# Kernel tuning notes

Measured on AMD Instinct MI355X. Metric: run time of the kernel, lower is better.

The kernel has to match this reference:

```python
import jax, jax.numpy as jnp
import numpy as np

N_NODES = 100000
N_EDGES = 1600000
H = 64
EPS_SM = 1e-16
NEG_SLOPE = 0.01  # LeakyReLU default
BN_EPS = 1e-5


def leaky_relu(x):
    return jnp.where(x >= 0, x, NEG_SLOPE * x)


def transformer_conv(x, src, tgt, edge_attr, Wq, bq, Wk, bk, Wv, bv, We, Ws, bs):
    # PyG TransformerConv, heads=1, concat=True, root_weight=True, lin_edge bias=False
    n = x.shape[0]
    q = x @ Wq + bq            # [N,H]
    k = x @ Wk + bk            # [N,H]
    v = x @ Wv + bv            # [N,H]
    e = edge_attr @ We         # [E,H]
    ke = k[src] + e            # [E,H]
    score = jnp.sum(q[tgt] * ke, axis=-1) / jnp.sqrt(jnp.float32(H))  # [E]
    # segment softmax over incoming edges of each target node
    m = jax.ops.segment_max(score, tgt, num_segments=n)
    m = jnp.where(jnp.isfinite(m), m, 0.0)
    p = jnp.exp(score - m[tgt])
    denom = jax.ops.segment_sum(p, tgt, num_segments=n)
    alpha = p / (denom[tgt] + EPS_SM)
    msg = (v[src] + e) * alpha[:, None]                  # [E,H]
    out = jax.ops.segment_sum(msg, tgt, num_segments=n)  # [N,H]
    return out + x @ Ws + bs


def batch_norm(x, gamma, beta):
    mean = jnp.mean(x, axis=0)
    var = jnp.mean((x - mean) ** 2, axis=0)
    return (x - mean) / jnp.sqrt(var + BN_EPS) * gamma + beta


def setup_inputs() -> dict:
    key = jax.random.key(0)
    ks = jax.random.split(key, 24)
    s = 0.05
    d = {
        "x": jax.random.normal(ks[0], (N_NODES, 2), jnp.float32),
        "edge_index": jax.random.randint(ks[1], (2, N_EDGES), 0, N_NODES, jnp.int32),
        "edge_attr": jax.random.normal(ks[2], (N_EDGES, 2), jnp.float32),
        "mask": jax.random.uniform(ks[3], (N_NODES,), jnp.float32),
        # gcn1 (in=2)
        "Wq1": jax.random.normal(ks[4], (2, H)) * s, "bq1": jnp.zeros((H,)),
        "Wk1": jax.random.normal(ks[5], (2, H)) * s, "bk1": jnp.zeros((H,)),
        "Wv1": jax.random.normal(ks[6], (2, H)) * s, "bv1": jnp.zeros((H,)),
        "We1": jax.random.normal(ks[7], (2, H)) * s,
        "Ws1": jax.random.normal(ks[8], (2, H)) * s, "bs1": jnp.zeros((H,)),
        # gcn2 (in=64)
        "Wq2": jax.random.normal(ks[9], (H, H)) * s, "bq2": jnp.zeros((H,)),
        "Wk2": jax.random.normal(ks[10], (H, H)) * s, "bk2": jnp.zeros((H,)),
        "Wv2": jax.random.normal(ks[11], (H, H)) * s, "bv2": jnp.zeros((H,)),
        "We2": jax.random.normal(ks[12], (2, H)) * s,
        "Ws2": jax.random.normal(ks[13], (H, H)) * s, "bs2": jnp.zeros((H,)),
        # batch norm
        "bn_gamma": jnp.ones((H,)), "bn_beta": jnp.zeros((H,)),
        # final MLP 64->32->1
        "Wf1": jax.random.normal(ks[14], (H, 32)) * s, "bf1": jnp.zeros((32,)),
        "Wf2": jax.random.normal(ks[15], (32, 1)) * s, "bf2": jnp.zeros((1,)),
        "iterations": 3,
    }
    return d


def reference(x, edge_index, edge_attr, mask,
              Wq1, bq1, Wk1, bk1, Wv1, bv1, We1, Ws1, bs1,
              Wq2, bq2, Wk2, bk2, Wv2, bv2, We2, Ws2, bs2,
              bn_gamma, bn_beta, Wf1, bf1, Wf2, bf2, iterations):
    src, tgt = edge_index[0], edge_index[1]
    h = transformer_conv(x, src, tgt, edge_attr, Wq1, bq1, Wk1, bk1, Wv1, bv1, We1, Ws1, bs1)
    h = leaky_relu(batch_norm(h, bn_gamma, bn_beta))
    h = leaky_relu(transformer_conv(h, src, tgt, edge_attr, Wq2, bq2, Wk2, bk2, Wv2, bv2, We2, Ws2, bs2))
    for _ in range(iterations - 1):
        h = leaky_relu(transformer_conv(h, src, tgt, edge_attr, Wq2, bq2, Wk2, bk2, Wv2, bv2, We2, Ws2, bs2))
    out = jnp.squeeze(leaky_relu(h @ Wf1 + bf1) @ Wf2 + bf2, axis=-1)  # [N]
    return out * mask
```

## Files before the change

kernel.cpp:

```cpp
#include <hip/hip_runtime.h>
#include <hip/hip_fp16.h>

#define N_NODES 100000
#define N_EDGES 1600000
#define SCAN_B ((N_NODES + 1023) / 1024)
#define BSHIFT 7
#define NB_BKT ((N_NODES + 127) / 128)
#define BCAP 2560

typedef _Float16 half2_t __attribute__((ext_vector_type(2)));
typedef _Float16 half8_t __attribute__((ext_vector_type(8)));
typedef float f32x4 __attribute__((ext_vector_type(4)));

__device__ __forceinline__ float lrelu(float x) { return x >= 0.f ? x : 0.01f * x; }

__global__ void k_count(const int* __restrict__ tgt, int* __restrict__ deg) {
    int i = blockIdx.x * 256 + threadIdx.x;
    atomicAdd(&deg[tgt[i]], 1);
}

__global__ void k_scan1(const int* __restrict__ deg, int* __restrict__ bsum) {
    __shared__ int s[256];
    int t = threadIdx.x;
    int gi = blockIdx.x * 1024 + t * 4;
    int v = 0;
    if (gi < N_NODES) {
        int4 d = *(const int4*)&deg[gi];
        v = d.x + d.y + d.z + d.w;
    }
    s[t] = v;
    __syncthreads();
    for (int d = 128; d > 0; d >>= 1) {
        if (t < d) s[t] += s[t + d];
        __syncthreads();
    }
    if (t == 0) bsum[blockIdx.x] = s[0];
}

__global__ void k_scan2(int* bsum, int* rowptr) {
    if (threadIdx.x == 0) {
        int run = 0;
        for (int b = 0; b < SCAN_B; b++) {
            int v = bsum[b];
            bsum[b] = run;
            run += v;
        }
        rowptr[N_NODES] = run;
    }
}

__global__ void k_scan3(const int* __restrict__ deg, const int* __restrict__ bsum,
                        int* __restrict__ rowptr, int* __restrict__ fill) {
    __shared__ int s[256];
    int t = threadIdx.x;
    int gi = blockIdx.x * 1024 + t * 4;
    int4 d = make_int4(0, 0, 0, 0);
    if (gi < N_NODES) d = *(const int4*)&deg[gi];
    int tsum = d.x + d.y + d.z + d.w;
    s[t] = tsum;
    __syncthreads();
    for (int dd = 1; dd < 256; dd <<= 1) {
        int val = (t >= dd) ? s[t - dd] : 0;
        __syncthreads();
        s[t] += val;
        __syncthreads();
    }
    int texcl = s[t] - tsum + bsum[blockIdx.x];
    if (gi < N_NODES) {
        int4 w;
        w.x = texcl;
        w.y = texcl + d.x;
        w.z = texcl + d.x + d.y;
        w.w = texcl + d.x + d.y + d.z;
        *(int4*)&rowptr[gi] = w;
        *(int4*)&fill[gi] = w;
    }
}

__global__ void k_scatter(const int* __restrict__ src, const int* __restrict__ tgt,
                          const float2* __restrict__ ea,
                          int* __restrict__ fill, int2* __restrict__ csr) {
    int i = blockIdx.x * 256 + threadIdx.x;
    int t = tgt[i];
    float2 e = ea[i];
    int pos = atomicAdd(&fill[t], 1);
    __half2 h2 = __floats2half2_rn(e.x, e.y);
    csr[pos] = make_int2(src[i], *(int*)&h2);
}

__global__ __launch_bounds__(256) void k_bin1(const int* __restrict__ src,
                                              const int* __restrict__ tgt,
                                              const float2* __restrict__ ea,
                                              int* __restrict__ gCur,
                                              int2* __restrict__ bin) {
    __shared__ int hist[NB_BKT];
    __shared__ int cur[NB_BKT];
    int tid = threadIdx.x;
    for (int b = tid; b < NB_BKT; b += 256) hist[b] = 0;
    __syncthreads();
    int base = blockIdx.x * 6400;
#pragma unroll 5
    for (int k = 0; k < 25; k++) {
        int i = base + k * 256 + tid;
        atomicAdd(&hist[tgt[i] >> BSHIFT], 1);
    }
    __syncthreads();
    for (int b = tid; b < NB_BKT; b += 256)
        cur[b] = atomicAdd(&gCur[b], hist[b]);
    __syncthreads();
    for (int k = 0; k < 25; k++) {
        int i = base + k * 256 + tid;
        int t = tgt[i];
        int b = t >> BSHIFT;
        float2 e = ea[i];
        int pos = atomicAdd(&cur[b], 1);
        if (pos < BCAP) {
            __half2 h2 = __floats2half2_rn(e.x, e.y);
            int2 rec;
            rec.x = src[i] | ((t & 127) << 20);
            rec.y = *(int*)&h2;
            bin[(size_t)b * BCAP + pos] = rec;
        }
    }
}

__global__ __launch_bounds__(256) void k_bin2(const int* __restrict__ gCnt,
                                              const int2* __restrict__ bin,
                                              int2* __restrict__ csr,
                                              int* __restrict__ fill) {
    __shared__ int cnt[128];
    int tid = threadIdx.x;
    if (tid < 128) cnt[tid] = 0;
    __syncthreads();
    int b = blockIdx.x;
    int nb = min(gCnt[b], BCAP);
    const int2* myb = &bin[(size_t)b * BCAP];
    for (int i = tid; i < nb; i += 256) {
        int2 rec = myb[i];
        int tloc = (rec.x >> 20) & 127;
        int s = rec.x & 0xFFFFF;
        int pos = atomicAdd(&cnt[tloc], 1);
        if (pos < 64) {
            int node = (b << BSHIFT) + tloc;
            csr[((size_t)node << 6) + pos] = make_int2(s | (rec.x & 0xFFF00000), rec.y);
        }
    }
    __syncthreads();
    if (tid < 128) {
        int node = (b << BSHIFT) + tid;
        if (node < N_NODES) fill[node] = min(cnt[tid], 64);
    }
}

__global__ void k_prep2(const float* __restrict__ Wq, const float* __restrict__ Wk,
                        const float* __restrict__ Ws, const float* __restrict__ We,
                        const float* __restrict__ bk, float* __restrict__ Wcomb) {
    int idx = blockIdx.x * 256 + threadIdx.x;
    if (idx >= 9216) return;
    int j = idx / 144;
    int m = idx - j * 144;
    float v = 0.f;
    if (m < 64) {
        float s = 0.f;
        for (int ch = 0; ch < 64; ch++) s += Wq[j * 64 + ch] * Wk[m * 64 + ch];
        v = 0.125f * s;
    } else if (m < 128) {
        v = Ws[j * 64 + (m - 64)];
    } else if (m == 128) {
        float s = 0.f;
        for (int ch = 0; ch < 64; ch++) s += Wq[j * 64 + ch] * bk[ch];
        v = 0.125f * s;
    } else if (m <= 130) {
        float s = 0.f;
        for (int ch = 0; ch < 64; ch++) s += Wq[j * 64 + ch] * We[(m - 129) * 64 + ch];
        v = 0.125f * s;
    }
    Wcomb[idx] = v;
}

__global__ void k_prepb(const float* __restrict__ Wk2, const float* __restrict__ We2,
                        const float* __restrict__ bq2, const float* __restrict__ bk2,
                        const float* __restrict__ bs2, const float* __restrict__ Wq1,
                        const float* __restrict__ Wk1, const float* __restrict__ We1,
                        const float* __restrict__ bq1, const float* __restrict__ bk1,
                        float* __restrict__ bcomb) {
    int t = threadIdx.x;
    if (t >= 160) return;
    float v = 0.f;
    if (t < 64) {
        float s = 0.f;
        for (int i = 0; i < 64; i++) s += Wk2[t * 64 + i] * bq2[i];
        v = 0.125f * s;
    } else if (t < 128) {
        v = bs2[t - 64];
    } else if (t == 128) {
        float s = 0.f;
        for (int i = 0; i < 64; i++) s += bq2[i] * bk2[i];
        v = 0.125f * s;
    } else if (t <= 130) {
        float s = 0.f;
        for (int i = 0; i < 64; i++) s += bq2[i] * We2[(t - 129) * 64 + i];
        v = 0.125f * s;
    } else if (t < 144) {
        v = 0.f;
    } else {
        int t2 = t - 144;
        float s = 0.f;
        if (t2 < 4) {
            int j = t2 >> 1, m = t2 & 1;
            for (int ch = 0; ch < 64; ch++) s += Wq1[j * 64 + ch] * Wk1[m * 64 + ch];
        } else if (t2 < 6) {
            int j = t2 - 4;
            for (int ch = 0; ch < 64; ch++) s += Wq1[j * 64 + ch] * bk1[ch];
        } else if (t2 < 8) {
            int m = t2 - 6;
            for (int ch = 0; ch < 64; ch++) s += bq1[ch] * Wk1[m * 64 + ch];
        } else if (t2 == 8) {
            for (int ch = 0; ch < 64; ch++) s += bq1[ch] * bk1[ch];
        } else if (t2 < 13) {
            int j = (t2 - 9) >> 1, d = (t2 - 9) & 1;
            for (int ch = 0; ch < 64; ch++) s += Wq1[j * 64 + ch] * We1[d * 64 + ch];
        } else if (t2 < 15) {
            int d = t2 - 13;
            for (int ch = 0; ch < 64; ch++) s += bq1[ch] * We1[d * 64 + ch];
        }
        v = 0.125f * s;
    }
    bcomb[t] = v;
}

__global__ void k_prepw(const float* __restrict__ Wcomb, __half* __restrict__ wp) {
    int t = blockIdx.x * 256 + threadIdx.x;
    if (t >= 9216) return;
    int e = t & 7;
    int lane = (t >> 3) & 63;
    int kh = (t >> 9) & 1;
    int fm = t >> 10;
    int k = (kh << 5) + ((lane >> 4) << 3) + e;
    int c = fm * 16 + (lane & 15);
    wp[t] = __float2half(Wcomb[k * 144 + c]);
}

__global__ void k_prepv(const float* __restrict__ Wv, __half* __restrict__ wvp) {
    int t = blockIdx.x * 256 + threadIdx.x;
    if (t >= 4096) return;
    int e = t & 7;
    int lane = (t >> 3) & 63;
    int kh = (t >> 9) & 1;
    int fm = t >> 10;
    int k = (kh << 5) + ((lane >> 4) << 3) + e;
    int c = fm * 16 + (lane & 15);
    wvp[t] = __float2half(Wv[k * 64 + c]);
}

__global__ __launch_bounds__(256) void k_agg1(
    const float* __restrict__ x, const int* __restrict__ idx,
    const int2* __restrict__ csr, const float* __restrict__ Wv,
    const float* __restrict__ We, const float* __restrict__ Ws,
    const float* __restrict__ bv, const float* __restrict__ bs,
    const float* __restrict__ prep, __half* __restrict__ oh, int bucket) {
    int node = blockIdx.x * 4 + (threadIdx.x >> 6);
    int lane = threadIdx.x & 63;
    float2 xt = *(const float2*)&x[(size_t)node << 1];
    float a0 = xt.x * prep[0] + xt.y * prep[2] + prep[6];
    float a1 = xt.x * prep[1] + xt.y * prep[3] + prep[7];
    float b1 = xt.x * prep[4] + xt.y * prep[5] + prep[8];
    float g0 = xt.x * prep[9] + xt.y * prep[11] + prep[13];
    float g1 = xt.x * prep[10] + xt.y * prep[12] + prep[14];

    float l = 0.f, px0 = 0.f, px1 = 0.f, pA = 0.f, pB = 0.f;
    if (bucket) {
        int deg = idx[node];
        bool valid = lane < deg;
        int2 rec = valid ? csr[((size_t)node << 6) + lane] : make_int2(0, 0);
        int src = rec.x & 0xFFFFF;
        float2 ef = __half22float2(*(__half2*)&rec.y);
        float2 xs = valid ? *(const float2*)&x[(size_t)src << 1] : make_float2(0.f, 0.f);
        float t = a0 * xs.x + a1 * xs.y + b1 + g0 * ef.x + g1 * ef.y;
        float pp = valid ? __expf(t) : 0.f;
        l = pp;
        px0 = pp * xs.x;
        px1 = pp * xs.y;
        pA = pp * ef.x;
        pB = pp * ef.y;
    } else {
        int beg = idx[node], end = idx[node + 1];
        for (int p = beg + lane; p < end; p += 64) {
            int2 rec = csr[p];
            float2 ef = __half22float2(*(__half2*)&rec.y);
            float2 xs = *(const float2*)&x[(size_t)rec.x << 1];
            float t = a0 * xs.x + a1 * xs.y + b1 + g0 * ef.x + g1 * ef.y;
            float pp = __expf(t);
            l += pp;
            px0 += pp * xs.x;
            px1 += pp * xs.y;
            pA += pp * ef.x;
            pB += pp * ef.y;
        }
    }
#pragma unroll
    for (int D = 1; D < 64; D <<= 1) {
        l += __shfl_xor(l, D, 64);
        px0 += __shfl_xor(px0, D, 64);
        px1 += __shfl_xor(px1, D, 64);
        pA += __shfl_xor(pA, D, 64);
        pB += __shfl_xor(pB, D, 64);
    }
    float inv = 1.f / (l + 1e-16f);
    int c = lane;
    float r = (px0 * Wv[c] + px1 * Wv[64 + c] + pA * We[c] + pB * We[64 + c] +
               l * bv[c]) * inv +
              xt.x * Ws[c] + xt.y * Ws[64 + c] + bs[c];
    oh[((size_t)node << 6) + c] = __float2half(r);
}

__global__ void k_bnp(const __half* __restrict__ oh, float* __restrict__ bnsum,
                      float* __restrict__ bnsq) {
    __shared__ float s1[256], s2[256];
    int t = threadIdx.x;
    int c = t & 63, nsub = t >> 6;
    float su = 0.f, sq = 0.f;
    int base = blockIdx.x * 400;
    for (int i = 0; i < 100; i++) {
        int node = base + i * 4 + nsub;
        float v = __half2float(oh[((size_t)node << 6) + c]);
        su += v;
        sq += v * v;
    }
    s1[t] = su;
    s2[t] = sq;
    __syncthreads();
    if (t < 64) {
        float a = s1[t] + s1[t + 64] + s1[t + 128] + s1[t + 192];
        float b = s2[t] + s2[t + 64] + s2[t + 128] + s2[t + 192];
        atomicAdd(&bnsum[t], a);
        atomicAdd(&bnsq[t], b);
    }
}

__global__ void k_bnf(const float* bnsum, const float* bnsq, const float* gamma,
                      const float* beta, float* bnab) {
    int c = threadIdx.x;
    float mean = bnsum[c] * (1.f / N_NODES);
    float var = bnsq[c] * (1.f / N_NODES) - mean * mean;
    float A = gamma[c] * rsqrtf(var + 1e-5f);
    bnab[c] = A;
    bnab[64 + c] = beta[c] - mean * A;
}

__global__ void k_bna(const __half* __restrict__ oh, const float* __restrict__ bnab,
                      __half* __restrict__ hh) {
    int idx = blockIdx.x * 256 + threadIdx.x;
    int c = idx & 63;
    float v = lrelu(__half2float(oh[idx]) * bnab[c] + bnab[64 + c]);
    hh[idx] = __float2half(v);
}

__global__ __launch_bounds__(256) void k_gemm(
    const __half* __restrict__ oh, const __half* __restrict__ hhin,
    const __half* __restrict__ wp, const float* __restrict__ bcomb,
    const float* __restrict__ bnab, int use_bn,
    __half* __restrict__ qh, float* __restrict__ ext, __half* __restrict__ hhout) {
    __shared__ __half qsm[64 * 68];
    int tid = threadIdx.x;
    int w = tid >> 6;
    int lane = tid & 63;
    int nloc = lane & 15;
    int kg = lane >> 4;
    int base = blockIdx.x * 64;

    half8_t A[2], AE[2];
    const half8_t* wpv = (const half8_t*)wp;
#pragma unroll
    for (int kh = 0; kh < 2; kh++) A[kh] = wpv[((w << 1) + kh) * 64 + lane];
    if (w == 3) {
#pragma unroll
        for (int kh = 0; kh < 2; kh++) AE[kh] = wpv[((8 << 1) + kh) * 64 + lane];
    }

    half8_t z8;
#pragma unroll
    for (int i = 0; i < 8; i++) z8[i] = (_Float16)0.f;

    half8_t B[4][2];
    int n[4];
    bool g[4];
#pragma unroll
    for (int nf = 0; nf < 4; nf++) {
        n[nf] = base + (nf << 4) + nloc;
        g[nf] = n[nf] < N_NODES;
    }

    if (use_bn) {
        float4 bnA[2][2], bnB[2][2];
#pragma unroll
        for (int kh = 0; kh < 2; kh++) {
            int k0 = (kh << 5) + (kg << 3);
            bnA[kh][0] = *(const float4*)&bnab[k0];
            bnA[kh][1] = *(const float4*)&bnab[k0 + 4];
            bnB[kh][0] = *(const float4*)&bnab[64 + k0];
            bnB[kh][1] = *(const float4*)&bnab[64 + k0 + 4];
        }
        const int4 zi4 = make_int4(0, 0, 0, 0);
#pragma unroll
        for (int nf = 0; nf < 4; nf++) {
            const __half* orow = oh + ((size_t)n[nf] << 6);
#pragma unroll
            for (int kh = 0; kh < 2; kh++) {
                int k0 = (kh << 5) + (kg << 3);
                int4 raw = g[nf] ? *(const int4*)&orow[k0] : zi4;
                const __half2* op = (const __half2*)&raw;
                float2 o01 = __half22float2(op[0]);
                float2 o23 = __half22float2(op[1]);
                float2 o45 = __half22float2(op[2]);
                float2 o67 = __half22float2(op[3]);
                float4 lo, hi;
                lo.x = lrelu(o01.x * bnA[kh][0].x + bnB[kh][0].x);
                lo.y = lrelu(o01.y * bnA[kh][0].y + bnB[kh][0].y);
                lo.z = lrelu(o23.x * bnA[kh][0].z + bnB[kh][0].z);
                lo.w = lrelu(o23.y * bnA[kh][0].w + bnB[kh][0].w);
                hi.x = lrelu(o45.x * bnA[kh][1].x + bnB[kh][1].x);
                hi.y = lrelu(o45.y * bnA[kh][1].y + bnB[kh][1].y);
                hi.z = lrelu(o67.x * bnA[kh][1].z + bnB[kh][1].z);
                hi.w = lrelu(o67.y * bnA[kh][1].w + bnB[kh][1].w);
                half8_t r;
                r[0] = (_Float16)lo.x; r[1] = (_Float16)lo.y;
                r[2] = (_Float16)lo.z; r[3] = (_Float16)lo.w;
                r[4] = (_Float16)hi.x; r[5] = (_Float16)hi.y;
                r[6] = (_Float16)hi.z; r[7] = (_Float16)hi.w;
                B[nf][kh] = r;
                if (g[nf]) *(half8_t*)&hhout[((size_t)n[nf] << 6) + k0] = r;
            }
        }
    } else {
#pragma unroll
        for (int nf = 0; nf < 4; nf++) {
#pragma unroll
            for (int kh = 0; kh < 2; kh++) {
                int k0 = (kh << 5) + (kg << 3);
                B[nf][kh] = g[nf] ? *(const half8_t*)&hhin[((size_t)n[nf] << 6) + k0]
                                  : z8;
            }
        }
    }

    f32x4 acc[4], accE[4];
#pragma unroll
    for (int nf = 0; nf < 4; nf++) {
        acc[nf] = (f32x4){0.f, 0.f, 0.f, 0.f};
        accE[nf] = (f32x4){0.f, 0.f, 0.f, 0.f};
    }

#pragma unroll
    for (int nf = 0; nf < 4; nf++) {
        acc[nf] = __builtin_amdgcn_mfma_f32_16x16x32_f16(A[0], B[nf][0], acc[nf],
                                                          0, 0, 0);
        acc[nf] = __builtin_amdgcn_mfma_f32_16x16x32_f16(A[1], B[nf][1], acc[nf],
                                                          0, 0, 0);
    }
    if (w == 3) {
#pragma unroll
        for (int nf = 0; nf < 4; nf++) {
            accE[nf] = __builtin_amdgcn_mfma_f32_16x16x32_f16(AE[0], B[nf][0],
                                                              accE[nf], 0, 0, 0);
            accE[nf] = __builtin_amdgcn_mfma_f32_16x16x32_f16(AE[1], B[nf][1],
                                                              accE[nf], 0, 0, 0);
        }
    }

    int rowg = kg << 2;
    int c0 = (w << 4) + rowg;
    float4 bi = *(const float4*)&bcomb[c0];
#pragma unroll
    for (int nf = 0; nf < 4; nf++) {
        int nl = (nf << 4) + nloc;
        __half2 p0 = __floats2half2_rn(acc[nf][0] + bi.x, acc[nf][1] + bi.y);
        __half2 p1 = __floats2half2_rn(acc[nf][2] + bi.z, acc[nf][3] + bi.w);
        *(__half2*)&qsm[nl * 68 + c0] = p0;
        *(__half2*)&qsm[nl * 68 + c0 + 2] = p1;
    }
    if (w == 3 && kg == 0) {
        float4 be = *(const float4*)&bcomb[128];
#pragma unroll
        for (int nf = 0; nf < 4; nf++) {
            if (!g[nf]) continue;
            float4 r;
            r.x = accE[nf][0] + be.x;
            r.y = accE[nf][1] + be.y;
            r.z = accE[nf][2] + be.z;
            r.w = accE[nf][3] + be.w;
            *(float4*)&ext[(size_t)n[nf] << 2] = r;
        }
    }
    __syncthreads();
#pragma unroll
    for (int rep = 0; rep < 8; rep++) {
        int i = rep * 256 + tid;
        int row = i >> 5;
        int col = (i & 31) << 1;
        if (base + row < N_NODES) {
            int v = *(int*)&qsm[row * 68 + col];
            *(int*)&qh[((size_t)(base + row) << 6) + col] = v;
        }
    }
}

__global__ __launch_bounds__(256) void k_fused(
    __half* qh, float* ext,
    const __half* __restrict__ hh_in, __half* __restrict__ hh_out,
    const int* __restrict__ idx, const int2* __restrict__ csr,
    const __half* __restrict__ wp, const __half* __restrict__ wvp,
    const float* __restrict__ We, const float* __restrict__ bv,
    const float* __restrict__ bcomb,
    const float* __restrict__ Wf1, const float* __restrict__ bf1,
    const float* __restrict__ Wf2, const float* __restrict__ bf2v,
    const float* __restrict__ mask, float* __restrict__ out,
    int last, int bucket) {
    __shared__ __align__(16) char smem[20480 + 9216 + 1024];
    float* red = (float*)smem;
    __half* rsm16 = (__half*)smem;
    float* rsm32 = (float*)smem;
    __half* Shatsm = (__half*)(smem + 20480);
    __half* qsm = (__half*)(smem + 20480);
    float* W1sm = (float*)(smem + 20480);
    float4* svecsm = (float4*)(smem + 20480 + 9216);

    int tid = threadIdx.x;
    int wv = tid >> 6;
    int lane = tid & 63;
    int base = blockIdx.x * 64;

    {
        int es = lane >> 2, cl = lane & 3;
        float* myred = &red[(wv * 64 + lane) * 20];
        int rb = wv * 64 * 20 + (lane >> 4) * 20 + (lane & 15);
        for (int nl = 0; nl < 16; nl++) {
            int node = base + (wv << 4) + nl;
            if (node >= N_NODES) continue;
            float4 ex = *(const float4*)&ext[(size_t)node << 2];
            float beta = ex.x, qe0 = ex.y, qe1 = ex.z;
            int4 qr0 = *(const int4*)&qh[((size_t)node << 6) + (cl << 4)];
            int4 qr1 = *(const int4*)&qh[((size_t)node << 6) + (cl << 4) + 8];
            const half2_t* qp0 = (const half2_t*)&qr0;
            const half2_t* qp1 = (const half2_t*)&qr1;

            float l = 0.f, sA = 0.f, sB = 0.f;
            float accv[16];
#pragma unroll
            for (int c = 0; c < 16; c++) accv[c] = 0.f;

            int nEdge, rbase2;
            if (bucket) {
                nEdge = idx[node];
                rbase2 = node << 6;
            } else {
                rbase2 = idx[node];
                nEdge = idx[node + 1] - rbase2;
            }
            int nIter = (nEdge + 15) >> 4;

            auto body = [&](int4 h0, int4 h1, int2 rec, bool ok) {
                const half2_t* hp0 = (const half2_t*)&h0;
                const half2_t* hp1 = (const half2_t*)&h1;
                float t = 0.f;
#if __has_builtin(__builtin_amdgcn_fdot2)
#pragma unroll
                for (int p = 0; p < 4; p++)
                    t = __builtin_amdgcn_fdot2(hp0[p], qp0[p], t, false);
#pragma unroll
                for (int p = 0; p < 4; p++)
                    t = __builtin_amdgcn_fdot2(hp1[p], qp1[p], t, false);
#else
                const __half* hq0 = (const __half*)&qr0;
                const __half* hq1 = (const __half*)&qr1;
                const __half* hh0 = (const __half*)&h0;
                const __half* hh1 = (const __half*)&h1;
#pragma unroll
                for (int c = 0; c < 8; c++)
                    t += __half2float(hh0[c]) * __half2float(hq0[c]);
#pragma unroll
                for (int c = 0; c < 8; c++)
                    t += __half2float(hh1[c]) * __half2float(hq1[c]);
#endif
                t += __shfl_xor(t, 1, 64);
                t += __shfl_xor(t, 2, 64);
                float2 ef = __half22float2(*(__half2*)&rec.y);
                t += beta + ef.x * qe0 + ef.y * qe1;
                float pp = ok ? __expf(t) : 0.f;
                l += pp;
                sA += pp * ef.x;
                sB += pp * ef.y;
                const __half* hs0 = (const __half*)&h0;
                const __half* hs1 = (const __half*)&h1;
#pragma unroll
                for (int c = 0; c < 8; c++) accv[c] += pp * __half2float(hs0[c]);
#pragma unroll
                for (int c = 0; c < 8; c++) accv[8 + c] += pp * __half2float(hs1[c]);
            };

            if (bucket) {
                int2 recs[4];
#pragma unroll
                for (int i = 0; i < 4; i++) {
                    int e = (i << 4) + es;
                    recs[i] = (e < nEdge) ? csr[(size_t)rbase2 + e] : make_int2(0, 0);
                }
                if (nIter > 0) {
                    int src0 = recs[0].x & 0xFFFFF;
                    const __half* hr = hh_in + ((size_t)src0 << 6) + (cl << 4);
                    int4 h0c = *(const int4*)&hr[0];
                    int4 h1c = *(const int4*)&hr[8];
#pragma unroll
                    for (int i = 0; i < 4; i++) {
                        if (i < nIter) {
                            int4 h0 = h0c, h1 = h1c;
                            if (i + 1 < nIter) {
                                int srcn = recs[i + 1].x & 0xFFFFF;
                                const __half* hrn =
                                    hh_in + ((size_t)srcn << 6) + (cl << 4);
                                h0c = *(const int4*)&hrn[0];
                                h1c = *(const int4*)&hrn[8];
                            }
                            body(h0, h1, recs[i], ((i << 4) + es) < nEdge);
                        }
                    }
                }
            } else {
                for (int i = 0; i < nIter; i++) {
                    int e = (i << 4) + es;
                    bool ok = e < nEdge;
                    int2 rec = ok ? csr[(size_t)rbase2 + e] : make_int2(0, 0);
                    int src = rec.x & 0xFFFFF;
                    const __half* hr = hh_in + ((size_t)src << 6) + (cl << 4);
                    int4 h0 = *(const int4*)&hr[0];
                    int4 h1 = *(const int4*)&hr[8];
                    body(h0, h1, rec, ok);
                }
            }

#pragma unroll
            for (int D = 4; D < 64; D <<= 1) {
                l += __shfl_xor(l, D, 64);
                sA += __shfl_xor(sA, D, 64);
                sB += __shfl_xor(sB, D, 64);
            }
            float inv = 1.f / (l + 1e-16f);

#pragma unroll
            for (int c = 0; c < 16; c += 4)
                *(float4*)&myred[c] =
                    make_float4(accv[c], accv[c + 1], accv[c + 2], accv[c + 3]);
            __asm__ volatile("" ::: "memory");
            float s = 0.f;
#pragma unroll
            for (int es2 = 0; es2 < 16; es2++) s += red[rb + es2 * 80];
            Shatsm[((wv << 4) + nl) * 72 + lane] = __float2half(s * inv);
            if (lane == 0)
                svecsm[(wv << 4) + nl] = make_float4(sA * inv, sB * inv, l * inv, 0.f);
            __asm__ volatile("" ::: "memory");
        }
    }
    __syncthreads();

    {
        int nloc = lane & 15, kg = lane >> 4;
        const half8_t* wvv = (const half8_t*)wvp;
        const half8_t* wpv = (const half8_t*)wp;
        half8_t Av0 = wvv[((wv << 1) + 0) * 64 + lane];
        half8_t Av1 = wvv[((wv << 1) + 1) * 64 + lane];
        half8_t As0 = wpv[(((4 + wv) << 1) + 0) * 64 + lane];
        half8_t As1 = wpv[(((4 + wv) << 1) + 1) * 64 + lane];

        int rowg = kg << 2;
        int c0 = (wv << 4) + rowg;
        float4 we0 = *(const float4*)&We[c0];
        float4 we1 = *(const float4*)&We[64 + c0];
        float4 bv4 = *(const float4*)&bv[c0];
        float4 bs4 = *(const float4*)&bcomb[64 + c0];

        half8_t z8;
#pragma unroll
        for (int i = 0; i < 8; i++) z8[i] = (_Float16)0.f;

#pragma unroll
        for (int nf = 0; nf < 4; nf++) {
            int n = base + (nf << 4) + nloc;
            bool g = n < N_NODES;
            int nl2 = (nf << 4) + nloc;
            const __half* srow = &Shatsm[nl2 * 72];
            const __half* hrow = hh_in + ((size_t)n << 6);
            half8_t Bs0 = g ? *(const half8_t*)&srow[kg << 3] : z8;
            half8_t Bs1 = g ? *(const half8_t*)&srow[32 + (kg << 3)] : z8;
            half8_t Bh0 = g ? *(const half8_t*)&hrow[kg << 3] : z8;
            half8_t Bh1 = g ? *(const half8_t*)&hrow[32 + (kg << 3)] : z8;

            f32x4 acc = (f32x4){0.f, 0.f, 0.f, 0.f};
            acc = __builtin_amdgcn_mfma_f32_16x16x32_f16(Av0, Bs0, acc, 0, 0, 0);
            acc = __builtin_amdgcn_mfma_f32_16x16x32_f16(Av1, Bs1, acc, 0, 0, 0);
            acc = __builtin_amdgcn_mfma_f32_16x16x32_f16(As0, Bh0, acc, 0, 0, 0);
            acc = __builtin_amdgcn_mfma_f32_16x16x32_f16(As1, Bh1, acc, 0, 0, 0);

            float4 sv = g ? svecsm[nl2] : make_float4(0.f, 0.f, 0.f, 0.f);
            float4 r;
            r.x = lrelu(acc[0] + sv.x * we0.x + sv.y * we1.x + sv.z * bv4.x + bs4.x);
            r.y = lrelu(acc[1] + sv.x * we0.y + sv.y * we1.y + sv.z * bv4.y + bs4.y);
            r.z = lrelu(acc[2] + sv.x * we0.z + sv.y * we1.z + sv.z * bv4.z + bs4.z);
            r.w = lrelu(acc[3] + sv.x * we0.w + sv.y * we1.w + sv.z * bv4.w + bs4.w);

            if (last) {
                *(float4*)&rsm32[nl2 * 68 + c0] = r;
            } else {
                __half2 p0 = __floats2half2_rn(r.x, r.y);
                __half2 p1 = __floats2half2_rn(r.z, r.w);
                *(__half2*)&rsm16[nl2 * 72 + c0] = p0;
                *(__half2*)&rsm16[nl2 * 72 + c0 + 2] = p1;
            }
        }
    }
    __syncthreads();

    if (!last) {
        int nloc = lane & 15, kg = lane >> 4;
        const half8_t* wpv = (const half8_t*)wp;
        half8_t A0 = wpv[((wv << 1) + 0) * 64 + lane];
        half8_t A1 = wpv[((wv << 1) + 1) * 64 + lane];
        half8_t AE0 = A0, AE1 = A1;
        if (wv == 3) {
            AE0 = wpv[16 * 64 + lane];
            AE1 = wpv[17 * 64 + lane];
        }
        int rowg = kg << 2;
        int c0 = (wv << 4) + rowg;
        float4 bi = *(const float4*)&bcomb[c0];

#pragma unroll
        for (int nf = 0; nf < 4; nf++) {
            int nl2 = (nf << 4) + nloc;
            const __half* rrow = &rsm16[nl2 * 72];
            half8_t B0 = *(const half8_t*)&rrow[kg << 3];
            half8_t B1 = *(const half8_t*)&rrow[32 + (kg << 3)];
            f32x4 acc = (f32x4){0.f, 0.f, 0.f, 0.f};
            acc = __builtin_amdgcn_mfma_f32_16x16x32_f16(A0, B0, acc, 0, 0, 0);
            acc = __builtin_amdgcn_mfma_f32_16x16x32_f16(A1, B1, acc, 0, 0, 0);
            __half2 p0 = __floats2half2_rn(acc[0] + bi.x, acc[1] + bi.y);
            __half2 p1 = __floats2half2_rn(acc[2] + bi.z, acc[3] + bi.w);
            *(__half2*)&qsm[nl2 * 72 + c0] = p0;
            *(__half2*)&qsm[nl2 * 72 + c0 + 2] = p1;
            if (wv == 3) {
                f32x4 ae = (f32x4){0.f, 0.f, 0.f, 0.f};
                ae = __builtin_amdgcn_mfma_f32_16x16x32_f16(AE0, B0, ae, 0, 0, 0);
                ae = __builtin_amdgcn_mfma_f32_16x16x32_f16(AE1, B1, ae, 0, 0, 0);
                if (kg == 0) {
                    int n = base + nl2;
                    if (n < N_NODES) {
                        float4 be = *(const float4*)&bcomb[128];
                        float4 r;
                        r.x = ae[0] + be.x;
                        r.y = ae[1] + be.y;
                        r.z = ae[2] + be.z;
                        r.w = ae[3] + be.w;
                        *(float4*)&ext[(size_t)n << 2] = r;
                    }
                }
            }
        }
        __syncthreads();
#pragma unroll
        for (int rep = 0; rep < 8; rep++) {
            int i = rep * 256 + tid;
            int row = i >> 5;
            int col = (i & 31) << 1;
            if (base + row < N_NODES) {
                *(int*)&qh[((size_t)(base + row) << 6) + col] =
                    *(int*)&qsm[row * 72 + col];
                *(int*)&hh_out[((size_t)(base + row) << 6) + col] =
                    *(int*)&rsm16[row * 72 + col];
            }
        }
    } else {
        for (int i = tid; i < 2048; i += 256) W1sm[i] = Wf1[i];
        __syncthreads();
        int nl2 = tid >> 2, jg = tid & 3;
        int node = base + nl2;
        float a8[8];
        const float* b1p = &bf1[jg << 3];
#pragma unroll
        for (int k = 0; k < 8; k++) a8[k] = b1p[k];
        const float* hr = &rsm32[nl2 * 68];
        for (int c = 0; c < 64; c++) {
            float hv = hr[c];
            const float* wr = &W1sm[(c << 5) + (jg << 3)];
            float4 wa = *(const float4*)&wr[0];
            float4 wb = *(const float4*)&wr[4];
            a8[0] += hv * wa.x; a8[1] += hv * wa.y;
            a8[2] += hv * wa.z; a8[3] += hv * wa.w;
            a8[4] += hv * wb.x; a8[5] += hv * wb.y;
            a8[6] += hv * wb.z; a8[7] += hv * wb.w;
        }
        const float* w2p = &Wf2[jg << 3];
        float zs = 0.f;
#pragma unroll
        for (int k = 0; k < 8; k++) zs += lrelu(a8[k]) * w2p[k];
        zs += __shfl_xor(zs, 1, 64);
        zs += __shfl_xor(zs, 2, 64);
        if (jg == 0 && node < N_NODES)
            out[node] = (zs + bf2v[0]) * mask[node];
    }
}

extern "C" void kernel_launch(void* const* d_in, const int* in_sizes, int n_in,
                              void* d_out, int out_size, void* d_ws, size_t ws_size,
                              hipStream_t stream) {
    const float* x = (const float*)d_in[0];
    const int* ei = (const int*)d_in[1];
    const float* ea = (const float*)d_in[2];
    const float* mask = (const float*)d_in[3];
    const float *Wq1 = (const float*)d_in[4], *bq1 = (const float*)d_in[5];
    const float *Wk1 = (const float*)d_in[6], *bk1 = (const float*)d_in[7];
    const float *Wv1 = (const float*)d_in[8], *bv1 = (const float*)d_in[9];
    const float *We1 = (const float*)d_in[10];
    const float *Ws1 = (const float*)d_in[11], *bs1 = (const float*)d_in[12];
    const float *Wq2 = (const float*)d_in[13], *bq2 = (const float*)d_in[14];
    const float *Wk2 = (const float*)d_in[15], *bk2 = (const float*)d_in[16];
    const float *Wv2 = (const float*)d_in[17], *bv2 = (const float*)d_in[18];
    const float *We2 = (const float*)d_in[19];
    const float *Ws2 = (const float*)d_in[20], *bs2 = (const float*)d_in[21];
    const float *gamma = (const float*)d_in[22], *beta = (const float*)d_in[23];
    const float *Wf1 = (const float*)d_in[24], *bf1 = (const float*)d_in[25];
    const float *Wf2 = (const float*)d_in[26], *bf2v = (const float*)d_in[27];
    float* out = (float*)d_out;

    const size_t bucket_need =
        (size_t)NB_BKT * BCAP * 8 + (size_t)N_NODES * 64 * 8 +
        (size_t)N_NODES * 64 * 2 * 4 +
        (size_t)N_NODES * 16 +
        (size_t)N_NODES * 4 * 3 + (1 << 20);
    bool use_bucket = ws_size >= bucket_need;

    char* ws = (char*)d_ws;
    size_t off = 0;
    auto alloc = [&](size_t b) {
        size_t r = off;
        off += (b + 255) & ~(size_t)255;
        return r;
    };
    int* deg = (int*)(ws + alloc(N_NODES * 4));
    int* fill = (int*)(ws + alloc(N_NODES * 4));
    int* rowptr = (int*)(ws + alloc((N_NODES + 1) * 4));
    int* bsum = (int*)(ws + alloc(SCAN_B * 4));
    int* gCur = (int*)(ws + alloc(NB_BKT * 4));
    float* bnsum = (float*)(ws + alloc(64 * 4));
    float* bnsq = (float*)(ws + alloc(64 * 4));
    float* bnab = (float*)(ws + alloc(128 * 4));
    float* Wcomb = (float*)(ws + alloc(9216 * 4));
    float* bcomb = (float*)(ws + alloc(160 * 4));
    __half* wp = (__half*)(ws + alloc(9216 * 2));
    __half* wvp = (__half*)(ws + alloc(4096 * 2));
    float* ext = (float*)(ws + alloc((size_t)N_NODES * 16));
    int2* bin1 = (int2*)(ws + alloc(use_bucket ? (size_t)NB_BKT * BCAP * 8 : 256));
    int2* csr = (int2*)(ws + alloc(use_bucket ? (size_t)N_NODES * 64 * 8
                                              : (size_t)N_EDGES * 8));
    __half* qh = (__half*)(ws + alloc((size_t)N_NODES * 64 * 2));
    __half* oh = (__half*)(ws + alloc((size_t)N_NODES * 64 * 2));
    __half* hh0 = (__half*)(ws + alloc((size_t)N_NODES * 64 * 2));
    __half* hh1 = (__half*)(ws + alloc((size_t)N_NODES * 64 * 2));

    const int* srcI = ei;
    const int* tgtI = ei + N_EDGES;

    hipMemsetAsync(bnsum, 0, 64 * 4, stream);
    hipMemsetAsync(bnsq, 0, 64 * 4, stream);

    k_prep2<<<36, 256, 0, stream>>>(Wq2, Wk2, Ws2, We2, bk2, Wcomb);
    k_prepb<<<1, 192, 0, stream>>>(Wk2, We2, bq2, bk2, bs2, Wq1, Wk1, We1, bq1, bk1,
                                   bcomb);
    k_prepw<<<36, 256, 0, stream>>>(Wcomb, wp);
    k_prepv<<<16, 256, 0, stream>>>(Wv2, wvp);

    const int* aggIdx;
    if (use_bucket) {
        hipMemsetAsync(gCur, 0, NB_BKT * 4, stream);
        k_bin1<<<250, 256, 0, stream>>>(srcI, tgtI, (const float2*)ea, gCur, bin1);
        k_bin2<<<NB_BKT, 256, 0, stream>>>(gCur, bin1, csr, fill);
        aggIdx = fill;
    } else {
        hipMemsetAsync(deg, 0, N_NODES * 4, stream);
        k_count<<<N_EDGES / 256, 256, 0, stream>>>(tgtI, deg);
        k_scan1<<<SCAN_B, 256, 0, stream>>>(deg, bsum);
        k_scan2<<<1, 64, 0, stream>>>(bsum, rowptr);
        k_scan3<<<SCAN_B, 256, 0, stream>>>(deg, bsum, rowptr, fill);
        k_scatter<<<N_EDGES / 256, 256, 0, stream>>>(srcI, tgtI, (const float2*)ea,
                                                     fill, csr);
        aggIdx = rowptr;
    }
    int bkt = use_bucket ? 1 : 0;

    k_agg1<<<N_NODES / 4, 256, 0, stream>>>(x, aggIdx, csr, Wv1, We1, Ws1, bv1, bs1,
                                            bcomb + 144, oh, bkt);
    k_bnp<<<250, 256, 0, stream>>>(oh, bnsum, bnsq);
    k_bnf<<<1, 64, 0, stream>>>(bnsum, bnsq, gamma, beta, bnab);
    if (!use_bucket)
        k_bna<<<N_NODES * 64 / 256, 256, 0, stream>>>(oh, bnab, hh0);

    const int gemm_grid = (N_NODES + 63) / 64;
    k_gemm<<<gemm_grid, 256, 0, stream>>>(oh, hh0, wp, bcomb, bnab, bkt, qh, ext,
                                          hh0);
    k_fused<<<gemm_grid, 256, 0, stream>>>(qh, ext, hh0, hh1, aggIdx, csr, wp, wvp,
                                           We2, bv2, bcomb, Wf1, bf1, Wf2, bf2v,
                                           mask, out, 0, bkt);
    k_fused<<<gemm_grid, 256, 0, stream>>>(qh, ext, hh1, hh0, aggIdx, csr, wp, wvp,
                                           We2, bv2, bcomb, Wf1, bf1, Wf2, bf2v,
                                           mask, out, 0, bkt);
    k_fused<<<gemm_grid, 256, 0, stream>>>(qh, ext, hh0, hh1, aggIdx, csr, wp, wvp,
                                           We2, bv2, bcomb, Wf1, bf1, Wf2, bf2v,
                                           mask, out, 1, bkt);
}
```

Before: 533.5 us.

## Replace LDS reduction with shuffle butterfly and template k_fused on LAST

The per-node cross-lane reduction of the 16 accumulators now uses a recursive-halving shuffle butterfly instead of a 20 KB shared-memory staging buffer. That shrinks the kernel's shared memory and lets the output column be derived from a bit-reversed lane index. k_fused is also templated on LAST, so the branch is resolved at compile time, the shared buffer is sized per variant, and launch bounds request 8 or 4 blocks per CU. The aim is higher occupancy and fewer LDS round-trips, at the cost of more shuffle instructions and possible register pressure or spills under the tighter launch bound.

```diff
diff --git a/kernel.cpp b/kernel.cpp
--- a/kernel.cpp
+++ b/kernel.cpp
@@ -505,7 +505,8 @@
     }
 }
 
-__global__ __launch_bounds__(256) void k_fused(
+template <int LAST>
+__global__ __launch_bounds__(256, LAST ? 4 : 8) void k_fused(
     __half* qh, float* ext,
     const __half* __restrict__ hh_in, __half* __restrict__ hh_out,
     const int* __restrict__ idx, const int2* __restrict__ csr,
@@ -515,15 +516,15 @@
     const float* __restrict__ Wf1, const float* __restrict__ bf1,
     const float* __restrict__ Wf2, const float* __restrict__ bf2v,
     const float* __restrict__ mask, float* __restrict__ out,
-    int last, int bucket) {
-    __shared__ __align__(16) char smem[20480 + 9216 + 1024];
-    float* red = (float*)smem;
+    int bucket) {
+    constexpr int RSM_BYTES = LAST ? (64 * 68 * 4) : (64 * 72 * 2);
+    __shared__ __align__(16) char smem[RSM_BYTES + 9216 + 1024];
     __half* rsm16 = (__half*)smem;
     float* rsm32 = (float*)smem;
-    __half* Shatsm = (__half*)(smem + 20480);
-    __half* qsm = (__half*)(smem + 20480);
-    float* W1sm = (float*)(smem + 20480);
-    float4* svecsm = (float4*)(smem + 20480 + 9216);
+    __half* Shatsm = (__half*)(smem + RSM_BYTES);
+    __half* qsm = (__half*)(smem + RSM_BYTES);
+    float* W1sm = (float*)(smem + RSM_BYTES);
+    float4* svecsm = (float4*)(smem + RSM_BYTES + 9216);
 
     int tid = threadIdx.x;
     int wv = tid >> 6;
@@ -532,8 +533,8 @@
 
     {
         int es = lane >> 2, cl = lane & 3;
-        float* myred = &red[(wv * 64 + lane) * 20];
-        int rb = wv * 64 * 20 + (lane >> 4) * 20 + (lane & 15);
+        int jf = ((es & 1) << 3) | ((es & 2) << 1) | ((es & 4) >> 1) | ((es & 8) >> 3);
+        int shatcol = (cl << 4) + jf;
         for (int nl = 0; nl < 16; nl++) {
             int node = base + (wv << 4) + nl;
             if (node >= N_NODES) continue;
@@ -647,17 +648,21 @@
             float inv = 1.f / (l + 1e-16f);
 
 #pragma unroll
-            for (int c = 0; c < 16; c += 4)
-                *(float4*)&myred[c] =
-                    make_float4(accv[c], accv[c + 1], accv[c + 2], accv[c + 3]);
-            __asm__ volatile("" ::: "memory");
-            float s = 0.f;
-#pragma unroll
-            for (int es2 = 0; es2 < 16; es2++) s += red[rb + es2 * 80];
-            Shatsm[((wv << 4) + nl) * 72 + lane] = __float2half(s * inv);
+            for (int step = 0; step < 4; step++) {
+                int m = 4 << step;
+                int half = 8 >> step;
+                bool up = (lane & m) != 0;
+#pragma unroll
+                for (int i = 0; i < half; i++) {
+                    float send = up ? accv[i] : accv[i + half];
+                    float recv = __shfl_xor(send, m, 64);
+                    float keep = up ? accv[i + half] : accv[i];
+                    accv[i] = keep + recv;
+                }
+            }
+            Shatsm[((wv << 4) + nl) * 72 + shatcol] = __float2half(accv[0] * inv);
             if (lane == 0)
                 svecsm[(wv << 4) + nl] = make_float4(sA * inv, sB * inv, l * inv, 0.f);
-            __asm__ volatile("" ::: "memory");
         }
     }
     __syncthreads();
@@ -707,7 +712,7 @@
             r.z = lrelu(acc[2] + sv.x * we0.z + sv.y * we1.z + sv.z * bv4.z + bs4.z);
             r.w = lrelu(acc[3] + sv.x * we0.w + sv.y * we1.w + sv.z * bv4.w + bs4.w);
 
-            if (last) {
+            if (LAST) {
                 *(float4*)&rsm32[nl2 * 68 + c0] = r;
             } else {
                 __half2 p0 = __floats2half2_rn(r.x, r.y);
@@ -719,7 +724,7 @@
     }
     __syncthreads();
 
-    if (!last) {
+    if (!LAST) {
         int nloc = lane & 15, kg = lane >> 4;
         const half8_t* wpv = (const half8_t*)wp;
         half8_t A0 = wpv[((wv << 1) + 0) * 64 + lane];
@@ -905,13 +910,13 @@
     const int gemm_grid = (N_NODES + 63) / 64;
     k_gemm<<<gemm_grid, 256, 0, stream>>>(oh, hh0, wp, bcomb, bnab, bkt, qh, ext,
                                           hh0);
-    k_fused<<<gemm_grid, 256, 0, stream>>>(qh, ext, hh0, hh1, aggIdx, csr, wp, wvp,
-                                           We2, bv2, bcomb, Wf1, bf1, Wf2, bf2v,
-                                           mask, out, 0, bkt);
-    k_fused<<<gemm_grid, 256, 0, stream>>>(qh, ext, hh1, hh0, aggIdx, csr, wp, wvp,
-                                           We2, bv2, bcomb, Wf1, bf1, Wf2, bf2v,
-                                           mask, out, 0, bkt);
-    k_fused<<<gemm_grid, 256, 0, stream>>>(qh, ext, hh0, hh1, aggIdx, csr, wp, wvp,
-                                           We2, bv2, bcomb, Wf1, bf1, Wf2, bf2v,
-                                           mask, out, 1, bkt);
-}
+    k_fused<0><<<gemm_grid, 256, 0, stream>>>(qh, ext, hh0, hh1, aggIdx, csr, wp,
+                                              wvp, We2, bv2, bcomb, Wf1, bf1, Wf2,
+                                              bf2v, mask, out, bkt);
+    k_fused<0><<<gemm_grid, 256, 0, stream>>>(qh, ext, hh1, hh0, aggIdx, csr, wp,
+                                              wvp, We2, bv2, bcomb, Wf1, bf1, Wf2,
+                                              bf2v, mask, out, bkt);
+    k_fused<1><<<gemm_grid, 256, 0, stream>>>(qh, ext, hh0, hh1, aggIdx, csr, wp,
+                                              wvp, We2, bv2, bcomb, Wf1, bf1, Wf2,
+                                              bf2v, mask, out, bkt);
+}
```

After: 612.5 us. 1.15x slower.
